# Performance work log

Hardware: AMD Instinct MI355X
Metric: run time of the kernel (lower is better)

The kernel has to match this reference:

```python
import jax, jax.numpy as jnp
import numpy as np

B, S, H = 32, 2048, 1024

def setup_inputs() -> dict:
    key = jax.random.key(0)
    k1, k2, k3, k4, k5 = jax.random.split(key, 5)
    return {
        "hidden": jax.random.normal(k1, (B, H), dtype=jnp.float32),
        "encoder_outputs": jax.random.normal(k2, (B, S, H), dtype=jnp.float32),
        "W_attn": jax.random.normal(k3, (H, H), dtype=jnp.float32) * (1.0 / np.sqrt(H)),
        "b_attn": jax.random.normal(k4, (H,), dtype=jnp.float32) * 0.01,
        "v": jax.random.uniform(k5, (H,), dtype=jnp.float32),
    }

def reference(hidden, encoder_outputs, W_attn, b_attn, v):
    # energy = tanh((enc + hidden[:,None,:]) @ W^T + b)  -> [B,S,H]
    x = encoder_outputs + hidden[:, None, :]
    energy = jnp.tanh(jnp.einsum('bsh,oh->bso', x, W_attn) + b_attn)
    scores = jnp.einsum('bsh,h->bs', energy, v)            # [B,S]
    attn_weights = jax.nn.softmax(scores, axis=1)          # [B,S]
    context = jnp.einsum('bs,bsh->bh', attn_weights, encoder_outputs)  # [B,H]
    return (context, attn_weights)
```

## Files before the change

### kernel.cpp

```cpp
#include <hip/hip_runtime.h>
#include <hip/hip_bf16.h>

#define BATCH 32
#define SEQ   2048
#define HID   1024
#define M_TOT (BATCH*SEQ)
#define NG    32

typedef __attribute__((ext_vector_type(8))) short          bf16x8;
typedef __attribute__((ext_vector_type(8))) unsigned short us8;
typedef __attribute__((ext_vector_type(4))) float          f32x4;

__device__ __forceinline__ unsigned short f2bf_rn(float x) {
    unsigned u = __float_as_uint(x);
    return (unsigned short)((u + 0x7fffu + ((u >> 16) & 1u)) >> 16);
}
__device__ __forceinline__ float bf2f(unsigned short h) {
    return __uint_as_float(((unsigned)h) << 16);
}
__device__ __forceinline__ unsigned cvt_pk_bf16(float s0, float s1) {
    unsigned r;
    asm("v_cvt_pk_bf16_f32 %0, %1, %2" : "=v"(r) : "v"(s0), "v"(s1));
    return r;
}

using as1_cv = const __attribute__((address_space(1))) void;
using as3_v  = __attribute__((address_space(3))) void;
__device__ __forceinline__ void gload16(const void* g, char* s) {
    __builtin_amdgcn_global_load_lds((as1_cv*)g, (as3_v*)s, 16, 0, 0);
}

#define FENCE() asm volatile("" ::: "memory")

#define MFMA_BLK(A4, B4, IB) do { \
  _Pragma("unroll") for (int i_ = 0; i_ < 4; i_++) \
  _Pragma("unroll") for (int j_ = 0; j_ < 4; j_++) \
    acc[(IB) + i_][j_] = __builtin_amdgcn_mfma_f32_16x16x32_bf16(A4[i_], B4[j_], acc[(IB)+i_][j_], 0, 0, 0); \
} while (0)

__global__ __launch_bounds__(256) void k_convW(const float* __restrict__ W,
                                               unsigned short* __restrict__ w2) {
    const int i8 = (blockIdx.x * 256 + threadIdx.x) * 8;
    const int o = i8 >> 10, h = i8 & 1023;
    float4 w0 = *(const float4*)(W + i8);
    float4 w1 = *(const float4*)(W + i8 + 4);
    float xs[8] = {w0.x, w0.y, w0.z, w0.w, w1.x, w1.y, w1.z, w1.w};
    us8 hv{}, lv{};
#pragma unroll
    for (int t = 0; t < 8; t++) {
        unsigned short xh = f2bf_rn(xs[t]);
        hv[t] = (unsigned short)xh;
        lv[t] = (unsigned short)f2bf_rn(xs[t] - bf2f(xh));
    }
    *(us8*)(w2 + (size_t)o * 2048 + h)        = hv;
    *(us8*)(w2 + (size_t)o * 2048 + 1024 + h) = lv;
}

__global__ __launch_bounds__(512, 2) void k_gemm_scores(
    const float* __restrict__ enc,
    const float* __restrict__ hidden,
    const unsigned short* __restrict__ w2,
    const float* __restrict__ b_attn,
    const float* __restrict__ v,
    float* __restrict__ pscore16)
{
    extern __shared__ char smem[];
    float* hidL = (float*)(smem + 131072);

    const int tid  = threadIdx.x;
    const int lane = tid & 63, wid = tid >> 6;
    const int wr = wid >> 2, wc = wid & 3;
    const int fr = lane & 15, g = lane >> 4;
    const int gxr = (fr >> 1) & 3;
    const int gsw = (g ^ gxr) * 16;

    const int bid  = blockIdx.x;
    const int swz  = (bid & 7) * 128 + (bid >> 3);
    const int mbase = (swz >> 2) * 256;
    const int nbase = (swz & 3) * 256;
    const int bidx  = mbase >> 11;

    const int arow = tid >> 1;
    const int acol = (tid & 1) * 16;
    const int axr  = (arow >> 1) & 3;
    const int ao0  = (((tid & 1) * 2) ^ axr) * 16;
    const int ao1  = ao0 ^ 16;
    const float* encP = enc + (size_t)(mbase + arow) * HID + acol;

    const int brow  = wid * 16 + (lane >> 2);
    const int bsx8  = ((lane & 3) ^ ((lane >> 3) & 3)) * 8;

    *(float2*)(hidL + tid * 2) = *(const float2*)(hidden + (size_t)bidx * HID + tid * 2);

    f32x4 acc[8][4];
#pragma unroll
    for (int i = 0; i < 8; i++)
#pragma unroll
        for (int j = 0; j < 4; j++) acc[i][j] = (f32x4)0.f;

    float4 er[4];

    auto loadEnc = [&](int Gn) {
        const float* ep = encP + Gn * 32;
#pragma unroll
        for (int q = 0; q < 4; q++) er[q] = *(const float4*)(ep + q * 4);
    };
    auto doConvA = [&](int Gn) {
        char* ap = smem + (Gn & 1) * 32768 + arow * 64;
        const float* hp = hidL + Gn * 32 + acol;
        unsigned hpk[8], lpk[8];
#pragma unroll
        for (int q = 0; q < 4; q++) {
            float4 e = er[q];
            float4 h = *(const float4*)(hp + q * 4);
            float x0 = e.x + h.x, x1 = e.y + h.y;
            float x2 = e.z + h.z, x3 = e.w + h.w;
            unsigned p01 = cvt_pk_bf16(x0, x1);
            unsigned p23 = cvt_pk_bf16(x2, x3);
            float h0 = __uint_as_float(p01 << 16);
            float h1 = __uint_as_float(p01 & 0xffff0000u);
            float h2 = __uint_as_float(p23 << 16);
            float h3 = __uint_as_float(p23 & 0xffff0000u);
            hpk[q * 2]     = p01;
            hpk[q * 2 + 1] = p23;
            lpk[q * 2]     = cvt_pk_bf16(x0 - h0, x1 - h1);
            lpk[q * 2 + 1] = cvt_pk_bf16(x2 - h2, x3 - h3);
        }
        *(uint4*)(ap + ao0)          = make_uint4(hpk[0], hpk[1], hpk[2], hpk[3]);
        *(uint4*)(ap + ao1)          = make_uint4(hpk[4], hpk[5], hpk[6], hpk[7]);
        *(uint4*)(ap + 16384 + ao0)  = make_uint4(lpk[0], lpk[1], lpk[2], lpk[3]);
        *(uint4*)(ap + 16384 + ao1)  = make_uint4(lpk[4], lpk[5], lpk[6], lpk[7]);
    };
    auto stageB = [&](int G2, int part) {
        const unsigned short* s0 = w2 + (size_t)(nbase + brow) * 2048 + part * 1024 + G2 * 32 + bsx8;
        char* d0 = smem + 65536 + (G2 & 1) * 32768 + part * 16384 + wid * 1024;
        gload16(s0, d0);
        gload16(s0 + (size_t)128 * 2048, d0 + 8192);
    };
    auto rdA = [&](int slot, int part, int i) -> bf16x8 {
        return *(const bf16x8*)(smem + slot * 32768 + part * 16384 +
                                (wr * 128 + i * 16 + fr) * 64 + gsw);
    };
    auto rdB = [&](int slot, int part, int j) -> bf16x8 {
        return *(const bf16x8*)(smem + 65536 + slot * 32768 + part * 16384 +
                                (wc * 64 + j * 16 + fr) * 64 + gsw);
    };

    loadEnc(0);
    stageB(0, 0); stageB(0, 1);
    asm volatile("s_waitcnt lgkmcnt(0)" ::: "memory");
    __builtin_amdgcn_s_barrier(); FENCE();
    doConvA(0);
    loadEnc(1);

    bf16x8 aa[4], aa2[4], bh[4], bl[4];

    for (int G = 0; G < NG; ++G) {
        const int slot = G & 1;
        asm volatile("s_waitcnt vmcnt(0) lgkmcnt(0)" ::: "memory");
        __builtin_amdgcn_s_barrier(); FENCE();

        if (G + 1 < NG) { stageB(G + 1, 0); stageB(G + 1, 1); }
#pragma unroll
        for (int j = 0; j < 4; j++) bh[j] = rdB(slot, 0, j);
#pragma unroll
        for (int i = 0; i < 4; i++) aa[i] = rdA(slot, 0, i);
        __builtin_amdgcn_s_setprio(1);
        MFMA_BLK(aa, bh, 0);
        __builtin_amdgcn_s_setprio(0);
#pragma unroll
        for (int j = 0; j < 4; j++) bl[j] = rdB(slot, 1, j);
        __builtin_amdgcn_s_setprio(1);
        MFMA_BLK(aa, bl, 0);
        __builtin_amdgcn_s_setprio(0);
#pragma unroll
        for (int i = 0; i < 4; i++) aa2[i] = rdA(slot, 0, 4 + i);
        __builtin_amdgcn_s_setprio(1);
        MFMA_BLK(aa2, bh, 4);
        MFMA_BLK(aa2, bl, 4);
        __builtin_amdgcn_s_setprio(0);
        if (G + 1 < NG) doConvA(G + 1);
        if (G + 2 < NG) loadEnc(G + 2);
#pragma unroll
        for (int i = 0; i < 4; i++) aa[i] = rdA(slot, 1, i);
        __builtin_amdgcn_s_setprio(1);
        MFMA_BLK(aa, bh, 0);
        __builtin_amdgcn_s_setprio(0);
#pragma unroll
        for (int i = 0; i < 4; i++) aa2[i] = rdA(slot, 1, 4 + i);
        __builtin_amdgcn_s_setprio(1);
        MFMA_BLK(aa2, bh, 4);
        __builtin_amdgcn_s_setprio(0);
    }

    float rs[8][4];
#pragma unroll
    for (int i = 0; i < 8; i++)
#pragma unroll
        for (int r = 0; r < 4; r++) rs[i][r] = 0.f;

#pragma unroll
    for (int j = 0; j < 4; j++) {
        const int n = nbase + wc * 64 + j * 16 + fr;
        const float ba = b_attn[n];
        const float vv = v[n];
#pragma unroll
        for (int i = 0; i < 8; i++)
#pragma unroll
            for (int r = 0; r < 4; r++) {
                float e  = acc[i][j][r] + ba;
                float ex = __expf(2.f * e);
                rs[i][r] += (1.f - 2.f / (ex + 1.f)) * vv;
            }
    }
#pragma unroll
    for (int off = 1; off < 16; off <<= 1)
#pragma unroll
        for (int i = 0; i < 8; i++)
#pragma unroll
            for (int r = 0; r < 4; r++) rs[i][r] += __shfl_xor(rs[i][r], off, 64);

    float v0 = 0.f, v1 = 0.f;
#pragma unroll
    for (int i = 0; i < 4; i++)
#pragma unroll
        for (int r = 0; r < 4; r++)
            if (fr == i * 4 + r) { v0 = rs[i][r]; v1 = rs[i + 4][r]; }

    const int plane = (swz & 3) * 4 + wc;
    const size_t pb = (size_t)plane * M_TOT + mbase + wr * 128 + g * 4 + (fr & 3);
    pscore16[pb + (fr >> 2) * 16]      = v0;
    pscore16[pb + (fr >> 2) * 16 + 64] = v1;
}

__global__ __launch_bounds__(256) void k_softmax(const float* __restrict__ ps,
                                                 float* __restrict__ out) {
    const int b = blockIdx.x, t = threadIdx.x;
    __shared__ float red[8];
    float loc[8];
    float lmax = -1e30f;
#pragma unroll
    for (int i = 0; i < 8; i++) {
        const int s = t + i * 256;
        float sc = 0.f;
#pragma unroll
        for (int p = 0; p < 16; p++) sc += ps[(size_t)p * M_TOT + (size_t)b * SEQ + s];
        loc[i] = sc;
        lmax = fmaxf(lmax, sc);
    }
    for (int o = 32; o; o >>= 1) lmax = fmaxf(lmax, __shfl_xor(lmax, o, 64));
    if ((t & 63) == 0) red[t >> 6] = lmax;
    __syncthreads();
    const float bmax = fmaxf(fmaxf(red[0], red[1]), fmaxf(red[2], red[3]));
    float ev[8], lsum = 0.f;
#pragma unroll
    for (int i = 0; i < 8; i++) { ev[i] = expf(loc[i] - bmax); lsum += ev[i]; }
    for (int o = 32; o; o >>= 1) lsum += __shfl_xor(lsum, o, 64);
    __syncthreads();
    if ((t & 63) == 0) red[4 + (t >> 6)] = lsum;
    __syncthreads();
    const float inv = 1.f / (red[4] + red[5] + red[6] + red[7]);
#pragma unroll
    for (int i = 0; i < 8; i++)
        out[(size_t)BATCH * HID + (size_t)b * SEQ + t + i * 256] = ev[i] * inv;
}

__global__ __launch_bounds__(256) void k_pctx(const float* __restrict__ enc,
                                              const float* __restrict__ attn,
                                              float* __restrict__ pctx) {
    const int hc = blockIdx.x, scb = blockIdx.y, b = blockIdx.z;
    const int h = hc * 256 + threadIdx.x;
    const float* ap = attn + (size_t)b * SEQ + scb * 256;
    const float* ep = enc + ((size_t)b * SEQ + scb * 256) * HID + h;
    float a = 0.f;
#pragma unroll 4
    for (int s = 0; s < 256; s++) a += ap[s] * ep[(size_t)s * HID];
    pctx[((size_t)scb * BATCH + b) * HID + h] = a;
}

__global__ __launch_bounds__(256) void k_ctx(const float* __restrict__ pctx,
                                             float* __restrict__ out) {
    const int i = blockIdx.x * 256 + threadIdx.x;
    float a = 0.f;
#pragma unroll
    for (int p = 0; p < 8; p++) a += pctx[(size_t)p * BATCH * HID + i];
    out[i] = a;
}

extern "C" void kernel_launch(void* const* d_in, const int* in_sizes, int n_in,
                              void* d_out, int out_size, void* d_ws, size_t ws_size,
                              hipStream_t stream) {
    const float* hidden = (const float*)d_in[0];
    const float* enc    = (const float*)d_in[1];
    const float* W      = (const float*)d_in[2];
    const float* b_attn = (const float*)d_in[3];
    const float* v      = (const float*)d_in[4];
    float* out = (float*)d_out;

    char* ws = (char*)d_ws;
    unsigned short* w2 = (unsigned short*)ws;
    float* pscore16    = (float*)(ws + ((size_t)4 << 20));
    float* pctx        = (float*)ws;

    const int smemBytes = 131072 + 4096;
    hipFuncSetAttribute((const void*)k_gemm_scores,
                        hipFuncAttributeMaxDynamicSharedMemorySize, smemBytes);

    k_convW<<<dim3(512), dim3(256), 0, stream>>>(W, w2);
    k_gemm_scores<<<dim3(1024), dim3(512), smemBytes, stream>>>(
        enc, hidden, w2, b_attn, v, pscore16);
    k_softmax<<<dim3(BATCH), dim3(256), 0, stream>>>(pscore16, out);
    k_pctx<<<dim3(4, 8, BATCH), dim3(256), 0, stream>>>(enc, out + BATCH * HID, pctx);
    k_ctx<<<dim3(128), dim3(256), 0, stream>>>(pctx, out);
}
```

Baseline: 444.3 us.

## Load encoder A-fragments directly into registers, bypassing LDS staging

Each wave now loads its own encoder rows from global memory straight into MFMA A-fragment registers (hi/lo bf16 split) instead of converting into shared memory and reading back. This removes the A-side LDS writes and reads and halves shared memory to allow higher occupancy. Conversion of the next K-step is interleaved with the low-part MFMAs. In exchange, global loads are uncoalesced per-lane (32-byte chunks per row) with less latency hiding, and register pressure grows from holding 16 fragments.

```diff
diff --git a/kernel.cpp b/kernel.cpp
--- a/kernel.cpp
+++ b/kernel.cpp
@@ -10,6 +10,7 @@
 typedef __attribute__((ext_vector_type(8))) short          bf16x8;
 typedef __attribute__((ext_vector_type(8))) unsigned short us8;
 typedef __attribute__((ext_vector_type(4))) float          f32x4;
+typedef __attribute__((ext_vector_type(4))) unsigned       u32x4;
 
 __device__ __forceinline__ unsigned short f2bf_rn(float x) {
     unsigned u = __float_as_uint(x);
@@ -31,12 +32,6 @@
 }
 
 #define FENCE() asm volatile("" ::: "memory")
-
-#define MFMA_BLK(A4, B4, IB) do { \
-  _Pragma("unroll") for (int i_ = 0; i_ < 4; i_++) \
-  _Pragma("unroll") for (int j_ = 0; j_ < 4; j_++) \
-    acc[(IB) + i_][j_] = __builtin_amdgcn_mfma_f32_16x16x32_bf16(A4[i_], B4[j_], acc[(IB)+i_][j_], 0, 0, 0); \
-} while (0)
 
 __global__ __launch_bounds__(256) void k_convW(const float* __restrict__ W,
                                                unsigned short* __restrict__ w2) {
@@ -65,7 +60,7 @@
     float* __restrict__ pscore16)
 {
     extern __shared__ char smem[];
-    float* hidL = (float*)(smem + 131072);
+    float* hidL = (float*)(smem + 65536);
 
     const int tid  = threadIdx.x;
     const int lane = tid & 63, wid = tid >> 6;
@@ -80,12 +75,7 @@
     const int nbase = (swz & 3) * 256;
     const int bidx  = mbase >> 11;
 
-    const int arow = tid >> 1;
-    const int acol = (tid & 1) * 16;
-    const int axr  = (arow >> 1) & 3;
-    const int ao0  = (((tid & 1) * 2) ^ axr) * 16;
-    const int ao1  = ao0 ^ 16;
-    const float* encP = enc + (size_t)(mbase + arow) * HID + acol;
+    const float* encBase = enc + (size_t)(mbase + wr * 128 + fr) * HID + g * 8;
 
     const int brow  = wid * 16 + (lane >> 2);
     const int bsx8  = ((lane & 3) ^ ((lane >> 3) & 3)) * 8;
@@ -98,62 +88,55 @@
 #pragma unroll
         for (int j = 0; j < 4; j++) acc[i][j] = (f32x4)0.f;
 
-    float4 er[4];
-
-    auto loadEnc = [&](int Gn) {
-        const float* ep = encP + Gn * 32;
-#pragma unroll
-        for (int q = 0; q < 4; q++) er[q] = *(const float4*)(ep + q * 4);
-    };
-    auto doConvA = [&](int Gn) {
-        char* ap = smem + (Gn & 1) * 32768 + arow * 64;
-        const float* hp = hidL + Gn * 32 + acol;
-        unsigned hpk[8], lpk[8];
-#pragma unroll
-        for (int q = 0; q < 4; q++) {
-            float4 e = er[q];
-            float4 h = *(const float4*)(hp + q * 4);
-            float x0 = e.x + h.x, x1 = e.y + h.y;
-            float x2 = e.z + h.z, x3 = e.w + h.w;
-            unsigned p01 = cvt_pk_bf16(x0, x1);
-            unsigned p23 = cvt_pk_bf16(x2, x3);
-            float h0 = __uint_as_float(p01 << 16);
-            float h1 = __uint_as_float(p01 & 0xffff0000u);
-            float h2 = __uint_as_float(p23 << 16);
-            float h3 = __uint_as_float(p23 & 0xffff0000u);
-            hpk[q * 2]     = p01;
-            hpk[q * 2 + 1] = p23;
-            lpk[q * 2]     = cvt_pk_bf16(x0 - h0, x1 - h1);
-            lpk[q * 2 + 1] = cvt_pk_bf16(x2 - h2, x3 - h3);
-        }
-        *(uint4*)(ap + ao0)          = make_uint4(hpk[0], hpk[1], hpk[2], hpk[3]);
-        *(uint4*)(ap + ao1)          = make_uint4(hpk[4], hpk[5], hpk[6], hpk[7]);
-        *(uint4*)(ap + 16384 + ao0)  = make_uint4(lpk[0], lpk[1], lpk[2], lpk[3]);
-        *(uint4*)(ap + 16384 + ao1)  = make_uint4(lpk[4], lpk[5], lpk[6], lpk[7]);
+    bf16x8 FH[8], FL[8], bh[4], bl[4];
+
+    auto convSet = [&](int i, int Gn, const float* hv) {
+        const float* ep = encBase + (size_t)(i * 16) * HID + Gn * 32;
+        float4 e0 = *(const float4*)ep;
+        float4 e1 = *(const float4*)(ep + 4);
+        float x0 = e0.x + hv[0], x1 = e0.y + hv[1];
+        float x2 = e0.z + hv[2], x3 = e0.w + hv[3];
+        float x4 = e1.x + hv[4], x5 = e1.y + hv[5];
+        float x6 = e1.z + hv[6], x7 = e1.w + hv[7];
+        unsigned h01 = cvt_pk_bf16(x0, x1);
+        unsigned h23 = cvt_pk_bf16(x2, x3);
+        unsigned h45 = cvt_pk_bf16(x4, x5);
+        unsigned h67 = cvt_pk_bf16(x6, x7);
+        unsigned l01 = cvt_pk_bf16(x0 - __uint_as_float(h01 << 16),
+                                   x1 - __uint_as_float(h01 & 0xffff0000u));
+        unsigned l23 = cvt_pk_bf16(x2 - __uint_as_float(h23 << 16),
+                                   x3 - __uint_as_float(h23 & 0xffff0000u));
+        unsigned l45 = cvt_pk_bf16(x4 - __uint_as_float(h45 << 16),
+                                   x5 - __uint_as_float(h45 & 0xffff0000u));
+        unsigned l67 = cvt_pk_bf16(x6 - __uint_as_float(h67 << 16),
+                                   x7 - __uint_as_float(h67 & 0xffff0000u));
+        union { u32x4 u; bf16x8 b; } H, L;
+        H.u[0] = h01; H.u[1] = h23; H.u[2] = h45; H.u[3] = h67;
+        L.u[0] = l01; L.u[1] = l23; L.u[2] = l45; L.u[3] = l67;
+        FH[i] = H.b;
+        FL[i] = L.b;
     };
     auto stageB = [&](int G2, int part) {
         const unsigned short* s0 = w2 + (size_t)(nbase + brow) * 2048 + part * 1024 + G2 * 32 + bsx8;
-        char* d0 = smem + 65536 + (G2 & 1) * 32768 + part * 16384 + wid * 1024;
+        char* d0 = smem + (G2 & 1) * 32768 + part * 16384 + wid * 1024;
         gload16(s0, d0);
         gload16(s0 + (size_t)128 * 2048, d0 + 8192);
     };
-    auto rdA = [&](int slot, int part, int i) -> bf16x8 {
+    auto rdB = [&](int slot, int part, int j) -> bf16x8 {
         return *(const bf16x8*)(smem + slot * 32768 + part * 16384 +
-                                (wr * 128 + i * 16 + fr) * 64 + gsw);
-    };
-    auto rdB = [&](int slot, int part, int j) -> bf16x8 {
-        return *(const bf16x8*)(smem + 65536 + slot * 32768 + part * 16384 +
                                 (wc * 64 + j * 16 + fr) * 64 + gsw);
     };
 
-    loadEnc(0);
     stageB(0, 0); stageB(0, 1);
     asm volatile("s_waitcnt lgkmcnt(0)" ::: "memory");
     __builtin_amdgcn_s_barrier(); FENCE();
-    doConvA(0);
-    loadEnc(1);
-
-    bf16x8 aa[4], aa2[4], bh[4], bl[4];
+    {
+        float hv[8];
+        *(float4*)&hv[0] = *(const float4*)(hidL + g * 8);
+        *(float4*)&hv[4] = *(const float4*)(hidL + g * 8 + 4);
+#pragma unroll
+        for (int i = 0; i < 8; i++) convSet(i, 0, hv);
+    }
 
     for (int G = 0; G < NG; ++G) {
         const int slot = G & 1;
@@ -164,33 +147,36 @@
 #pragma unroll
         for (int j = 0; j < 4; j++) bh[j] = rdB(slot, 0, j);
 #pragma unroll
-        for (int i = 0; i < 4; i++) aa[i] = rdA(slot, 0, i);
+        for (int j = 0; j < 4; j++) bl[j] = rdB(slot, 1, j);
+
         __builtin_amdgcn_s_setprio(1);
-        MFMA_BLK(aa, bh, 0);
+#pragma unroll
+        for (int i = 0; i < 8; i++)
+#pragma unroll
+            for (int j = 0; j < 4; j++)
+                acc[i][j] = __builtin_amdgcn_mfma_f32_16x16x32_bf16(FH[i], bh[j], acc[i][j], 0, 0, 0);
+#pragma unroll
+        for (int i = 0; i < 8; i++)
+#pragma unroll
+            for (int j = 0; j < 4; j++)
+                acc[i][j] = __builtin_amdgcn_mfma_f32_16x16x32_bf16(FH[i], bl[j], acc[i][j], 0, 0, 0);
         __builtin_amdgcn_s_setprio(0);
-#pragma unroll
-        for (int j = 0; j < 4; j++) bl[j] = rdB(slot, 1, j);
-        __builtin_amdgcn_s_setprio(1);
-        MFMA_BLK(aa, bl, 0);
-        __builtin_amdgcn_s_setprio(0);
-#pragma unroll
-        for (int i = 0; i < 4; i++) aa2[i] = rdA(slot, 0, 4 + i);
-        __builtin_amdgcn_s_setprio(1);
-        MFMA_BLK(aa2, bh, 4);
-        MFMA_BLK(aa2, bl, 4);
-        __builtin_amdgcn_s_setprio(0);
-        if (G + 1 < NG) doConvA(G + 1);
-        if (G + 2 < NG) loadEnc(G + 2);
-#pragma unroll
-        for (int i = 0; i < 4; i++) aa[i] = rdA(slot, 1, i);
-        __builtin_amdgcn_s_setprio(1);
-        MFMA_BLK(aa, bh, 0);
-        __builtin_amdgcn_s_setprio(0);
-#pragma unroll
-        for (int i = 0; i < 4; i++) aa2[i] = rdA(slot, 1, 4 + i);
-        __builtin_amdgcn_s_setprio(1);
-        MFMA_BLK(aa2, bh, 4);
-        __builtin_amdgcn_s_setprio(0);
+
+        float hv[8];
+        if (G + 1 < NG) {
+            *(float4*)&hv[0] = *(const float4*)(hidL + (G + 1) * 32 + g * 8);
+            *(float4*)&hv[4] = *(const float4*)(hidL + (G + 1) * 32 + g * 8 + 4);
+        }
+
+#pragma unroll
+        for (int i = 0; i < 8; i++) {
+            __builtin_amdgcn_s_setprio(1);
+#pragma unroll
+            for (int j = 0; j < 4; j++)
+                acc[i][j] = __builtin_amdgcn_mfma_f32_16x16x32_bf16(FL[i], bh[j], acc[i][j], 0, 0, 0);
+            __builtin_amdgcn_s_setprio(0);
+            if (G + 1 < NG) convSet(i, G + 1, hv);
+        }
     }
 
     float rs[8][4];
@@ -302,7 +288,7 @@
     float* pscore16    = (float*)(ws + ((size_t)4 << 20));
     float* pctx        = (float*)ws;
 
-    const int smemBytes = 131072 + 4096;
+    const int smemBytes = 65536 + 4096;
     hipFuncSetAttribute((const void*)k_gemm_scores,
                         hipFuncAttributeMaxDynamicSharedMemorySize, smemBytes);
 
```

New measurement: 753.1 us. 1.7x slower.
